# Performance work log

Measured on AMD Instinct MI355X. Metric: run time of the kernel, lower is better.

## Reference

```python
import jax, jax.numpy as jnp
import numpy as np

N_QUBITS = 10
DEPTH = 3
KSIZE = 16
DILATION = 1
NFREQ = 8

I4 = np.eye(4, dtype=np.complex64)
XX4 = np.fliplr(np.eye(4)).astype(np.complex64)
YY4 = np.array([[0, 0, 0, -1], [0, 0, 1, 0], [0, 1, 0, 0], [-1, 0, 0, 0]], dtype=np.complex64)


def _u3(t, p, l):
    ct = jnp.cos(t / 2).astype(jnp.complex64)
    st = jnp.sin(t / 2).astype(jnp.complex64)
    ep, el = jnp.exp(1j * p), jnp.exp(1j * l)
    return jnp.stack([jnp.stack([ct, -el * st]), jnp.stack([ep * st, ep * el * ct])])


def _ising_zz(t):
    em, ep = jnp.exp(-0.5j * t), jnp.exp(0.5j * t)
    return jnp.diag(jnp.stack([em, ep, ep, em]))


def _ising_xx(t):
    return jnp.cos(t / 2) * I4 - 1j * jnp.sin(t / 2) * XX4


def _ising_yy(t):
    return jnp.cos(t / 2) * I4 - 1j * jnp.sin(t / 2) * YY4


def _cu3(t, p, l):
    # controlled-U3 (control = 1): deferred-measurement form of qml.cond(measure, U3)
    return jnp.eye(4, dtype=jnp.complex64).at[2:, 2:].set(_u3(t, p, l))


def _apply_1q(state, U, wire):
    s = jnp.moveaxis(state, 1 + wire, -1)
    if U.ndim == 3:  # per-sample gate (batched angles)
        s = jnp.einsum('bij,b...j->b...i', U, s)
    else:
        s = jnp.einsum('ij,...j->...i', U, s)
    return jnp.moveaxis(s, -1, 1 + wire)


def _apply_2q(state, U, w1, w2):
    s = jnp.moveaxis(state, (1 + w1, 1 + w2), (-2, -1))
    shp = s.shape
    s = s.reshape(shp[:-2] + (4,))
    s = jnp.einsum('ij,...j->...i', U, s)
    return jnp.moveaxis(s.reshape(shp), (-2, -1), (1 + w1, 1 + w2))


def _run_circuit(angles, freq_scale, conv_params, pool_params):
    Bm = angles.shape[0]
    state = jnp.zeros((Bm, 2 ** N_QUBITS), jnp.complex64).at[:, 0].set(1.0)
    state = state.reshape((Bm,) + (2,) * N_QUBITS)
    # frequency-matched encoding: RY(a) then RX(freq_scale * a), per-sample angles
    for i in range(N_QUBITS):
        a = angles[:, i]
        c = jnp.cos(a / 2).astype(jnp.complex64)
        s = jnp.sin(a / 2).astype(jnp.complex64)
        ry = jnp.stack([jnp.stack([c, -s], -1), jnp.stack([s, c], -1)], -2)
        state = _apply_1q(state, ry, i)
        b = freq_scale[i] * a
        cb = jnp.cos(b / 2).astype(jnp.complex64)
        sb = jnp.sin(b / 2).astype(jnp.complex64)
        rx = jnp.stack([jnp.stack([cb, -1j * sb], -1), jnp.stack([-1j * sb, cb], -1)], -2)
        state = _apply_1q(state, rx, i)
    wires = list(range(N_QUBITS))
    for layer in range(DEPTH):
        wp = conv_params[layer]
        nw = len(wires)
        for parity in (0, 1):
            for i2, w in enumerate(wires):
                if i2 % 2 == parity and i2 < nw - 1:
                    nxt = wires[i2 + 1]
                    state = _apply_1q(state, _u3(wp[i2, 0], wp[i2, 1], wp[i2, 2]), w)
                    state = _apply_1q(state, _u3(wp[i2 + 1, 3], wp[i2 + 1, 4], wp[i2 + 1, 5]), nxt)
                    state = _apply_2q(state, _ising_zz(wp[i2, 6]), w, nxt)
                    state = _apply_2q(state, _ising_yy(wp[i2, 7]), w, nxt)
                    state = _apply_2q(state, _ising_xx(wp[i2, 8]), w, nxt)
                    state = _apply_1q(state, _u3(wp[i2, 9], wp[i2, 10], wp[i2, 11]), w)
                    state = _apply_1q(state, _u3(wp[i2 + 1, 12], wp[i2 + 1, 13], wp[i2 + 1, 14]), nxt)
        pp = pool_params[layer]
        for i2, w in enumerate(wires):
            if i2 % 2 == 1:
                state = _apply_2q(state, _cu3(pp[i2 // 2, 0], pp[i2 // 2, 1], pp[i2 // 2, 2]), w, wires[i2 - 1])
        wires = wires[::2]
    p = jnp.abs(state) ** 2
    p = p.reshape(Bm, 2, -1).sum(-1)
    return p[:, 0] - p[:, 1]  # <Z_0>


def _forward(x, proj_w, proj_b, freq_scale, conv_params, pool_params, agg_weights):
    B, C, T = x.shape
    eff = DILATION * (KSIZE - 1)
    W = T - eff
    idx = jnp.arange(W)[:, None] + DILATION * jnp.arange(KSIZE)[None, :]  # [W,K]
    win = x[:, :, idx]  # [B,C,W,K]
    f = jnp.fft.rfft(win, axis=-1)[..., :NFREQ]  # [B,C,W,NF]
    feats = jnp.stack([jnp.log1p(jnp.abs(f)), jnp.angle(f) / jnp.pi], -1)  # [B,C,W,NF,2]
    feats = jnp.transpose(feats, (0, 2, 1, 3, 4)).reshape(B, W, -1)  # [B,W,C*NF*2]
    proj = jnp.tanh(feats @ proj_w.T + proj_b) * jnp.pi  # [B,W,n_qubits]
    ev = _run_circuit(proj.reshape(B * W, N_QUBITS), freq_scale, conv_params, pool_params)
    outs = ev.reshape(B, W)
    wts = jax.nn.softmax(agg_weights[:W])
    return (outs * wts[None, :]).sum(1)


def setup_inputs():
    key = jax.random.key(0)
    k = jax.random.split(key, 6)
    fft_dim = 22 * NFREQ * 2
    return {
        'x': jax.random.normal(k[0], (16, 22, 128), jnp.float32),
        'proj_w': jax.random.normal(k[1], (N_QUBITS, fft_dim), jnp.float32) / np.sqrt(fft_dim).astype(np.float32),
        'proj_b': jnp.zeros((N_QUBITS,), jnp.float32),
        'freq_scale': jnp.linspace(0.5, 3.0, N_QUBITS, dtype=jnp.float32),
        'conv_params': 0.1 * jax.random.normal(k[2], (DEPTH, N_QUBITS, 15), jnp.float32),
        'pool_params': 0.1 * jax.random.normal(k[3], (DEPTH, N_QUBITS // 2, 3), jnp.float32),
        'agg_weights': jnp.zeros((113,), jnp.float32),
    }


def reference(x, proj_w, proj_b, freq_scale, conv_params, pool_params, agg_weights):
    return _forward(x, proj_w, proj_b, freq_scale, conv_params, pool_params, agg_weights)
```

## Files before the change

### kernel.cpp

```cpp
#include <hip/hip_runtime.h>
#include <math.h>

#define NQ 10
#define NSTATE 1024
#define WW 113
#define BB 16
#define CC 22
#define KK 16
#define NF 8
#define FDIM 352
#define NS (BB*WW)
#define NGATE 23
#define SL(j) ((j) ^ (((j) >> 5) & 31))

__device__ __forceinline__ float2 cmul(float2 a, float2 b) {
    return make_float2(a.x*b.x - a.y*b.y, a.x*b.y + a.y*b.x);
}

__constant__ int G_KIND[NGATE]  = {0,0,0,0,0, 0,0,0,0, 1,1,1,1,1, 0,0,0,0, 1,1, 0,0, 1};
__constant__ int G_LAYER[NGATE] = {0,0,0,0,0, 0,0,0,0, 0,0,0,0,0, 1,1,1,1, 1,1, 2,2, 2};
__constant__ int G_IA[NGATE]    = {0,2,4,6,8, 1,3,5,7, 0,1,2,3,4, 0,2,1,3, 0,1, 0,1, 0};

__device__ void u3mat(float2* U, float th, float ph, float lm) {
    float ct, st, cp, sp, cl, sl;
    sincosf(th * 0.5f, &st, &ct);
    sincosf(ph, &sp, &cp);
    sincosf(lm, &sl, &cl);
    U[0] = make_float2(ct, 0.f);
    U[1] = make_float2(-cl * st, -sl * st);
    U[2] = make_float2(cp * st, sp * st);
    U[3] = make_float2((cp * cl - sp * sl) * ct, (sp * cl + cp * sl) * ct);
}

__device__ void mm4(float2* C, const float2* A, const float2* B) {
#pragma unroll
    for (int i = 0; i < 4; ++i)
#pragma unroll
        for (int j = 0; j < 4; ++j) {
            float2 acc = make_float2(0.f, 0.f);
#pragma unroll
            for (int k = 0; k < 4; ++k) {
                float2 p = cmul(A[i*4+k], B[k*4+j]);
                acc.x += p.x; acc.y += p.y;
            }
            C[i*4+j] = acc;
        }
}

__global__ __launch_bounds__(64) void prep_kernel(
    const float* __restrict__ conv,
    const float* __restrict__ pool,
    const float* __restrict__ aggw,
    float2* __restrict__ mats,
    float* __restrict__ wts,
    float* __restrict__ out)
{
    const int t = threadIdx.x;

    float a0 = (t < WW) ? aggw[t] : -1e30f;
    float a1 = (t + 64 < WW) ? aggw[t + 64] : -1e30f;
    float mx = fmaxf(a0, a1);
    for (int off = 32; off > 0; off >>= 1) mx = fmaxf(mx, __shfl_xor(mx, off));
    float e0 = (t < WW) ? expf(a0 - mx) : 0.f;
    float e1 = (t + 64 < WW) ? expf(a1 - mx) : 0.f;
    float es = e0 + e1;
    for (int off = 32; off > 0; off >>= 1) es += __shfl_xor(es, off);
    float inv = 1.0f / es;
    if (t < WW) wts[t] = e0 * inv;
    if (t + 64 < WW) wts[t + 64] = e1 * inv;
    if (t < BB) out[t] = 0.f;

    if (t >= NGATE) return;
    int kind = G_KIND[t], layer = G_LAYER[t], ia = G_IA[t];
    float2 F[16];
    if (kind == 0) {
        const float* wp = conv + layer * 150;
        float2 Uw0[4], Un0[4], Uw1[4], Un1[4];
        u3mat(Uw0, wp[ia*15+0], wp[ia*15+1], wp[ia*15+2]);
        u3mat(Un0, wp[(ia+1)*15+3], wp[(ia+1)*15+4], wp[(ia+1)*15+5]);
        u3mat(Uw1, wp[ia*15+9], wp[ia*15+10], wp[ia*15+11]);
        u3mat(Un1, wp[(ia+1)*15+12], wp[(ia+1)*15+13], wp[(ia+1)*15+14]);
        float2 Kpre[16], Kpost[16];
#pragma unroll
        for (int a = 0; a < 2; ++a)
#pragma unroll
        for (int b = 0; b < 2; ++b)
#pragma unroll
        for (int c = 0; c < 2; ++c)
#pragma unroll
        for (int d = 0; d < 2; ++d) {
            Kpre [(2*a+b)*4 + (2*c+d)] = cmul(Uw0[a*2+c], Un0[b*2+d]);
            Kpost[(2*a+b)*4 + (2*c+d)] = cmul(Uw1[a*2+c], Un1[b*2+d]);
        }
        float cz, sz, cy, sy, cx, sx;
        sincosf(wp[ia*15+6] * 0.5f, &sz, &cz);
        sincosf(wp[ia*15+7] * 0.5f, &sy, &cy);
        sincosf(wp[ia*15+8] * 0.5f, &sx, &cx);
        float2 Z[16], Y[16], X[16];
#pragma unroll
        for (int k = 0; k < 16; ++k) { Z[k] = make_float2(0,0); Y[k] = make_float2(0,0); X[k] = make_float2(0,0); }
        Z[0]  = make_float2(cz, -sz); Z[5]  = make_float2(cz, sz);
        Z[10] = make_float2(cz,  sz); Z[15] = make_float2(cz, -sz);
        Y[0] = Y[5] = Y[10] = Y[15] = make_float2(cy, 0);
        Y[0*4+3] = make_float2(0,  sy); Y[1*4+2] = make_float2(0, -sy);
        Y[2*4+1] = make_float2(0, -sy); Y[3*4+0] = make_float2(0,  sy);
        X[0] = X[5] = X[10] = X[15] = make_float2(cx, 0);
        X[0*4+3] = X[1*4+2] = X[2*4+1] = X[3*4+0] = make_float2(0, -sx);
        float2 T1[16], M[16], T2[16];
        mm4(T1, Y, Z);
        mm4(M, X, T1);
        mm4(T2, M, Kpre);
        mm4(F, Kpost, T2);
    } else {
        const float* pp = pool + layer * 15 + ia * 3;
        float2 U[4];
        u3mat(U, pp[0], pp[1], pp[2]);
#pragma unroll
        for (int k = 0; k < 16; ++k) F[k] = make_float2(0,0);
        F[0*4+0] = make_float2(1,0); F[1*4+1] = make_float2(1,0);
        F[2*4+2] = U[0]; F[2*4+3] = U[1];
        F[3*4+2] = U[2]; F[3*4+3] = U[3];
    }
#pragma unroll
    for (int k = 0; k < 16; ++k) mats[t*16 + k] = F[k];
}

template<int PW, int PN>
__device__ __forceinline__ void gate2q(float2* st, const float2* __restrict__ m, int tid)
{
    constexpr int PL = (PW < PN) ? PW : PN;
    constexpr int PH = (PW < PN) ? PN : PW;
    int t1   = ((tid >> PL) << (PL + 1)) | (tid & ((1 << PL) - 1));
    int base = ((t1  >> PH) << (PH + 1)) | (t1  & ((1 << PH) - 1));
    const int i0 = SL(base);
    const int i1 = SL(base | (1 << PN));
    const int i2 = SL(base | (1 << PW));
    const int i3 = SL(base | (1 << PW) | (1 << PN));
    float2 a[4];
    a[0] = st[i0]; a[1] = st[i1]; a[2] = st[i2]; a[3] = st[i3];
    float2 n[4];
#pragma unroll
    for (int g = 0; g < 4; ++g) {
        float accx = 0.f, accy = 0.f;
#pragma unroll
        for (int h = 0; h < 4; ++h) {
            float2 mm = m[g*4 + h];
            accx = fmaf(mm.x, a[h].x, accx);
            accx = fmaf(-mm.y, a[h].y, accx);
            accy = fmaf(mm.x, a[h].y, accy);
            accy = fmaf(mm.y, a[h].x, accy);
        }
        n[g] = make_float2(accx, accy);
    }
    st[i0] = n[0]; st[i1] = n[1]; st[i2] = n[2]; st[i3] = n[3];
}

__global__ __launch_bounds__(256) void fused_kernel(
    const float* __restrict__ x,
    const float* __restrict__ proj_w,
    const float* __restrict__ proj_b,
    const float* __restrict__ freq_scale,
    const float2* __restrict__ mats,
    const float* __restrict__ wts,
    float* __restrict__ out)
{
    const int s = blockIdx.x;
    const int b = s / WW, w = s % WW;
    const int tid = threadIdx.x;

    __shared__ float2 st[NSTATE];
    __shared__ float twre[16], twim[16];
    __shared__ float angs[NQ];
    __shared__ float2 vq[2 * NQ];
    __shared__ float part[4];

    float* win  = (float*)st;
    float* feat = (float*)st + 512;

    for (int e = tid; e < CC * KK; e += 256) {
        int c = e >> 4, n = e & 15;
        win[e] = x[b * (CC * 128) + c * 128 + w + n];
    }
    if (tid < 16) {
        float ang = -(float)M_PI * (float)tid / 8.0f;
        twre[tid] = cosf(ang);
        twim[tid] = sinf(ang);
    }
    __syncthreads();

    float fval = 0.f, fval2 = 0.f;
    if (tid < CC * NF) {
        int c = tid >> 3, k = tid & 7;
        float re = 0.f, im = 0.f;
#pragma unroll
        for (int n = 0; n < 16; ++n) {
            int m = (k * n) & 15;
            float xv = win[c * 16 + n];
            re += xv * twre[m];
            im += xv * twim[m];
        }
        fval  = log1pf(sqrtf(re * re + im * im));
        fval2 = atan2f(im, re) * (float)(1.0 / M_PI);
    }
    __syncthreads();
    if (tid < CC * NF) {
        int c = tid >> 3, k = tid & 7;
        feat[c * 16 + k * 2]     = fval;
        feat[c * 16 + k * 2 + 1] = fval2;
    }
    __syncthreads();

    {
        int v = tid >> 6, lane = tid & 63;
        for (int q = v; q < NQ; q += 4) {
            float acc = 0.f;
            for (int e = lane; e < FDIM; e += 64) acc += feat[e] * proj_w[q * FDIM + e];
            for (int off = 32; off > 0; off >>= 1) acc += __shfl_xor(acc, off);
            if (lane == 0) angs[q] = tanhf(acc + proj_b[q]) * (float)M_PI;
        }
    }
    __syncthreads();

    if (tid < NQ) {
        float a = angs[tid];
        float bf = freq_scale[tid] * a;
        float ca, sa, cb, sb;
        sincosf(a * 0.5f, &sa, &ca);
        sincosf(bf * 0.5f, &sb, &cb);
        vq[2 * tid]     = make_float2(cb * ca, -sb * sa);
        vq[2 * tid + 1] = make_float2(cb * sa, -sb * ca);
    }
    __syncthreads();

    for (int idx = tid; idx < NSTATE; idx += 256) {
        float r = 1.f, i = 0.f;
#pragma unroll
        for (int q = 0; q < NQ; ++q) {
            int bit = (idx >> (9 - q)) & 1;
            float2 vv = vq[2 * q + bit];
            float nr = r * vv.x - i * vv.y;
            float ni = r * vv.y + i * vv.x;
            r = nr; i = ni;
        }
        st[SL(idx)] = make_float2(r, i);
    }
    __syncthreads();

#define GATE(G, PW, PN) gate2q<PW, PN>(st, mats + (G)*16, tid); __syncthreads();
    GATE(0, 9, 8) GATE(1, 7, 6) GATE(2, 5, 4) GATE(3, 3, 2) GATE(4, 1, 0)
    GATE(5, 8, 7) GATE(6, 6, 5) GATE(7, 4, 3) GATE(8, 2, 1)
    GATE(9, 8, 9) GATE(10, 6, 7) GATE(11, 4, 5) GATE(12, 2, 3) GATE(13, 0, 1)
    GATE(14, 9, 7) GATE(15, 5, 3) GATE(16, 7, 5) GATE(17, 3, 1)
    GATE(18, 7, 9) GATE(19, 3, 5)
    GATE(20, 9, 5) GATE(21, 5, 1)
    GATE(22, 5, 9)
#undef GATE

    float local = 0.f;
    for (int idx = tid; idx < NSTATE; idx += 256) {
        float2 am = st[idx];
        float p = am.x * am.x + am.y * am.y;
        local += (idx < 512) ? p : -p;
    }
    for (int off = 32; off > 0; off >>= 1) local += __shfl_xor(local, off);
    if ((tid & 63) == 0) part[tid >> 6] = local;
    __syncthreads();
    if (tid == 0) {
        float ev = part[0] + part[1] + part[2] + part[3];
        atomicAdd(&out[b], ev * wts[w]);
    }
}

extern "C" void kernel_launch(void* const* d_in, const int* in_sizes, int n_in,
                              void* d_out, int out_size, void* d_ws, size_t ws_size,
                              hipStream_t stream)
{
    const float* x           = (const float*)d_in[0];
    const float* proj_w      = (const float*)d_in[1];
    const float* proj_b      = (const float*)d_in[2];
    const float* freq_scale  = (const float*)d_in[3];
    const float* conv_params = (const float*)d_in[4];
    const float* pool_params = (const float*)d_in[5];
    const float* aggw        = (const float*)d_in[6];
    float* out = (float*)d_out;

    float2* mats = (float2*)d_ws;
    float* wts   = (float*)d_ws + NGATE * 16 * 2;

    prep_kernel<<<1, 64, 0, stream>>>(conv_params, pool_params, aggw, mats, wts, out);
    fused_kernel<<<NS, 256, 0, stream>>>(x, proj_w, proj_b, freq_scale, mats, wts, out);
}
```

Measured before the change: 112.0 us.

## Specialize controlled pooling gates and parallelize gate-matrix prep per element

Pooling gates are controlled-U3, so they now touch only the two amplitudes where the control bit is set, which halves shared-memory traffic and arithmetic for those gates. The gate-matrix prep kernel now uses one thread per matrix element, with a closed-form product, instead of one thread per gate doing several 4x4 matrix multiplies. Swizzled index offsets are derived by XOR instead of being recomputed, and the DFT uses fma. Block count and sync structure are unchanged, so the gain is limited to the gate phase and prep latency.

```diff
diff --git a/kernel.cpp b/kernel.cpp
--- a/kernel.cpp
+++ b/kernel.cpp
@@ -6,22 +6,31 @@
 #define WW 113
 #define BB 16
 #define CC 22
-#define KK 16
 #define NF 8
 #define FDIM 352
 #define NS (BB*WW)
 #define NGATE 23
-#define SL(j) ((j) ^ (((j) >> 5) & 31))
-
-__device__ __forceinline__ float2 cmul(float2 a, float2 b) {
+
+__device__ __forceinline__ constexpr int SLOT(int j) { return j ^ ((j >> 5) & 31); }
+__device__ __forceinline__ constexpr int DD(int p) { return (1 << p) | (p >= 5 ? (1 << (p - 5)) : 0); }
+
+__device__ __forceinline__ int ins0(int j, int p) {
+    return ((j >> p) << (p + 1)) | (j & ((1 << p) - 1));
+}
+
+__device__ __forceinline__ float2 cmulf(float2 a, float2 b) {
     return make_float2(a.x*b.x - a.y*b.y, a.x*b.y + a.y*b.x);
+}
+__device__ __forceinline__ void cmacf(float2& acc, float2 c, float2 v) {
+    acc.x = fmaf(c.x, v.x, acc.x); acc.x = fmaf(-c.y, v.y, acc.x);
+    acc.y = fmaf(c.x, v.y, acc.y); acc.y = fmaf(c.y, v.x, acc.y);
 }
 
 __constant__ int G_KIND[NGATE]  = {0,0,0,0,0, 0,0,0,0, 1,1,1,1,1, 0,0,0,0, 1,1, 0,0, 1};
 __constant__ int G_LAYER[NGATE] = {0,0,0,0,0, 0,0,0,0, 0,0,0,0,0, 1,1,1,1, 1,1, 2,2, 2};
 __constant__ int G_IA[NGATE]    = {0,2,4,6,8, 1,3,5,7, 0,1,2,3,4, 0,2,1,3, 0,1, 0,1, 0};
 
-__device__ void u3mat(float2* U, float th, float ph, float lm) {
+__device__ __forceinline__ void u3mat(float2* U, float th, float ph, float lm) {
     float ct, st, cp, sp, cl, sl;
     sincosf(th * 0.5f, &st, &ct);
     sincosf(ph, &sp, &cp);
@@ -32,22 +41,7 @@
     U[3] = make_float2((cp * cl - sp * sl) * ct, (sp * cl + cp * sl) * ct);
 }
 
-__device__ void mm4(float2* C, const float2* A, const float2* B) {
-#pragma unroll
-    for (int i = 0; i < 4; ++i)
-#pragma unroll
-        for (int j = 0; j < 4; ++j) {
-            float2 acc = make_float2(0.f, 0.f);
-#pragma unroll
-            for (int k = 0; k < 4; ++k) {
-                float2 p = cmul(A[i*4+k], B[k*4+j]);
-                acc.x += p.x; acc.y += p.y;
-            }
-            C[i*4+j] = acc;
-        }
-}
-
-__global__ __launch_bounds__(64) void prep_kernel(
+__global__ __launch_bounds__(384) void prep_kernel(
     const float* __restrict__ conv,
     const float* __restrict__ pool,
     const float* __restrict__ aggw,
@@ -57,102 +51,105 @@
 {
     const int t = threadIdx.x;
 
-    float a0 = (t < WW) ? aggw[t] : -1e30f;
-    float a1 = (t + 64 < WW) ? aggw[t + 64] : -1e30f;
-    float mx = fmaxf(a0, a1);
-    for (int off = 32; off > 0; off >>= 1) mx = fmaxf(mx, __shfl_xor(mx, off));
-    float e0 = (t < WW) ? expf(a0 - mx) : 0.f;
-    float e1 = (t + 64 < WW) ? expf(a1 - mx) : 0.f;
-    float es = e0 + e1;
-    for (int off = 32; off > 0; off >>= 1) es += __shfl_xor(es, off);
-    float inv = 1.0f / es;
-    if (t < WW) wts[t] = e0 * inv;
-    if (t + 64 < WW) wts[t + 64] = e1 * inv;
-    if (t < BB) out[t] = 0.f;
-
-    if (t >= NGATE) return;
-    int kind = G_KIND[t], layer = G_LAYER[t], ia = G_IA[t];
-    float2 F[16];
-    if (kind == 0) {
+    if (t < 64) {
+        float a0 = (t < WW) ? aggw[t] : -1e30f;
+        float a1 = (t + 64 < WW) ? aggw[t + 64] : -1e30f;
+        float mx = fmaxf(a0, a1);
+        for (int off = 32; off > 0; off >>= 1) mx = fmaxf(mx, __shfl_xor(mx, off));
+        float e0 = (t < WW) ? expf(a0 - mx) : 0.f;
+        float e1 = (t + 64 < WW) ? expf(a1 - mx) : 0.f;
+        float es = e0 + e1;
+        for (int off = 32; off > 0; off >>= 1) es += __shfl_xor(es, off);
+        float inv = 1.0f / es;
+        if (t < WW) wts[t] = e0 * inv;
+        if (t + 64 < WW) wts[t + 64] = e1 * inv;
+        if (t < BB) out[t] = 0.f;
+    }
+
+    if (t >= NGATE * 16) return;
+    const int g = t >> 4, k = t & 15;
+    const int i = k >> 2, j = k & 3;
+    const int kind = G_KIND[g], layer = G_LAYER[g], ia = G_IA[g];
+    float2 F;
+    if (kind == 1) {
+        const float* pp = pool + layer * 15 + ia * 3;
+        if (i < 2 || j < 2) {
+            F = (i == j) ? make_float2(1.f, 0.f) : make_float2(0.f, 0.f);
+        } else {
+            float2 U[4];
+            u3mat(U, pp[0], pp[1], pp[2]);
+            F = U[(i - 2) * 2 + (j - 2)];
+        }
+    } else {
         const float* wp = conv + layer * 150;
         float2 Uw0[4], Un0[4], Uw1[4], Un1[4];
-        u3mat(Uw0, wp[ia*15+0], wp[ia*15+1], wp[ia*15+2]);
-        u3mat(Un0, wp[(ia+1)*15+3], wp[(ia+1)*15+4], wp[(ia+1)*15+5]);
-        u3mat(Uw1, wp[ia*15+9], wp[ia*15+10], wp[ia*15+11]);
+        u3mat(Uw0, wp[ia*15+0],  wp[ia*15+1],  wp[ia*15+2]);
+        u3mat(Un0, wp[(ia+1)*15+3],  wp[(ia+1)*15+4],  wp[(ia+1)*15+5]);
+        u3mat(Uw1, wp[ia*15+9],  wp[ia*15+10], wp[ia*15+11]);
         u3mat(Un1, wp[(ia+1)*15+12], wp[(ia+1)*15+13], wp[(ia+1)*15+14]);
-        float2 Kpre[16], Kpost[16];
-#pragma unroll
-        for (int a = 0; a < 2; ++a)
-#pragma unroll
-        for (int b = 0; b < 2; ++b)
-#pragma unroll
-        for (int c = 0; c < 2; ++c)
-#pragma unroll
-        for (int d = 0; d < 2; ++d) {
-            Kpre [(2*a+b)*4 + (2*c+d)] = cmul(Uw0[a*2+c], Un0[b*2+d]);
-            Kpost[(2*a+b)*4 + (2*c+d)] = cmul(Uw1[a*2+c], Un1[b*2+d]);
-        }
         float cz, sz, cy, sy, cx, sx;
         sincosf(wp[ia*15+6] * 0.5f, &sz, &cz);
         sincosf(wp[ia*15+7] * 0.5f, &sy, &cy);
         sincosf(wp[ia*15+8] * 0.5f, &sx, &cx);
-        float2 Z[16], Y[16], X[16];
-#pragma unroll
-        for (int k = 0; k < 16; ++k) { Z[k] = make_float2(0,0); Y[k] = make_float2(0,0); X[k] = make_float2(0,0); }
-        Z[0]  = make_float2(cz, -sz); Z[5]  = make_float2(cz, sz);
-        Z[10] = make_float2(cz,  sz); Z[15] = make_float2(cz, -sz);
-        Y[0] = Y[5] = Y[10] = Y[15] = make_float2(cy, 0);
-        Y[0*4+3] = make_float2(0,  sy); Y[1*4+2] = make_float2(0, -sy);
-        Y[2*4+1] = make_float2(0, -sy); Y[3*4+0] = make_float2(0,  sy);
-        X[0] = X[5] = X[10] = X[15] = make_float2(cx, 0);
-        X[0*4+3] = X[1*4+2] = X[2*4+1] = X[3*4+0] = make_float2(0, -sx);
-        float2 T1[16], M[16], T2[16];
-        mm4(T1, Y, Z);
-        mm4(M, X, T1);
-        mm4(T2, M, Kpre);
-        mm4(F, Kpost, T2);
-    } else {
-        const float* pp = pool + layer * 15 + ia * 3;
-        float2 U[4];
-        u3mat(U, pp[0], pp[1], pp[2]);
-#pragma unroll
-        for (int k = 0; k < 16; ++k) F[k] = make_float2(0,0);
-        F[0*4+0] = make_float2(1,0); F[1*4+1] = make_float2(1,0);
-        F[2*4+2] = U[0]; F[2*4+3] = U[1];
-        F[3*4+2] = U[2]; F[3*4+3] = U[3];
-    }
-#pragma unroll
-    for (int k = 0; k < 16; ++k) mats[t*16 + k] = F[k];
+        float2 acc = make_float2(0.f, 0.f);
+#pragma unroll
+        for (int a = 0; a < 4; ++a) {
+            const float sa = (a == 0 || a == 3) ? 1.f : -1.f;
+            const float2 za = (a == 0 || a == 3) ? make_float2(cz, -sz)
+                                                 : make_float2(cz,  sz);
+            const float daa = fmaf(sa * sx, sy, cx * cy);
+            const float oaa = fmaf(sa * sy, cx, -sx * cy);
+            float2 Mdiag = make_float2(daa * za.x, daa * za.y);
+            float2 Moff  = make_float2(-oaa * za.y, oaa * za.x);
+            float2 kpost = cmulf(Uw1[(i >> 1) * 2 + (a >> 1)], Un1[(i & 1) * 2 + (a & 1)]);
+            float2 kpreA = cmulf(Uw0[(a >> 1) * 2 + (j >> 1)], Un0[(a & 1) * 2 + (j & 1)]);
+            float2 kpreN = cmulf(Uw0[(1 - (a >> 1)) * 2 + (j >> 1)], Un0[(1 - (a & 1)) * 2 + (j & 1)]);
+            float2 inner = cmulf(Mdiag, kpreA);
+            cmacf(inner, Moff, kpreN);
+            cmacf(acc, kpost, inner);
+        }
+        F = acc;
+    }
+    mats[g * 16 + k] = F;
 }
 
 template<int PW, int PN>
-__device__ __forceinline__ void gate2q(float2* st, const float2* __restrict__ m, int tid)
+__device__ __forceinline__ void conv2q(float2* st, const float2* __restrict__ m, int tid)
 {
     constexpr int PL = (PW < PN) ? PW : PN;
     constexpr int PH = (PW < PN) ? PN : PW;
     int t1   = ((tid >> PL) << (PL + 1)) | (tid & ((1 << PL) - 1));
     int base = ((t1  >> PH) << (PH + 1)) | (t1  & ((1 << PH) - 1));
-    const int i0 = SL(base);
-    const int i1 = SL(base | (1 << PN));
-    const int i2 = SL(base | (1 << PW));
-    const int i3 = SL(base | (1 << PW) | (1 << PN));
-    float2 a[4];
-    a[0] = st[i0]; a[1] = st[i1]; a[2] = st[i2]; a[3] = st[i3];
+    const int i0 = SLOT(base);
+    const int i1 = i0 ^ DD(PN);
+    const int i2 = i0 ^ DD(PW);
+    const int i3 = i2 ^ DD(PN);
+    float2 a0 = st[i0], a1 = st[i1], a2 = st[i2], a3 = st[i3];
     float2 n[4];
 #pragma unroll
     for (int g = 0; g < 4; ++g) {
-        float accx = 0.f, accy = 0.f;
-#pragma unroll
-        for (int h = 0; h < 4; ++h) {
-            float2 mm = m[g*4 + h];
-            accx = fmaf(mm.x, a[h].x, accx);
-            accx = fmaf(-mm.y, a[h].y, accx);
-            accy = fmaf(mm.x, a[h].y, accy);
-            accy = fmaf(mm.y, a[h].x, accy);
-        }
-        n[g] = make_float2(accx, accy);
+        float2 acc = cmulf(m[g*4+0], a0);
+        cmacf(acc, m[g*4+1], a1);
+        cmacf(acc, m[g*4+2], a2);
+        cmacf(acc, m[g*4+3], a3);
+        n[g] = acc;
     }
     st[i0] = n[0]; st[i1] = n[1]; st[i2] = n[2]; st[i3] = n[3];
+}
+
+template<int PC, int PT>
+__device__ __forceinline__ void pool2q(float2* st, const float2* __restrict__ m, int tid)
+{
+    constexpr int PL = (PC < PT) ? PC : PT;
+    constexpr int PH = (PC < PT) ? PT : PC;
+    int t1   = ((tid >> PL) << (PL + 1)) | (tid & ((1 << PL) - 1));
+    int base = ((t1  >> PH) << (PH + 1)) | (t1  & ((1 << PH) - 1));
+    const int i2 = SLOT(base) ^ DD(PC);
+    const int i3 = i2 ^ DD(PT);
+    float2 a2 = st[i2], a3 = st[i3];
+    float2 n2 = cmulf(m[10], a2); cmacf(n2, m[11], a3);
+    float2 n3 = cmulf(m[14], a2); cmacf(n3, m[15], a3);
+    st[i2] = n2; st[i3] = n3;
 }
 
 __global__ __launch_bounds__(256) void fused_kernel(
@@ -177,14 +174,14 @@
     float* win  = (float*)st;
     float* feat = (float*)st + 512;
 
-    for (int e = tid; e < CC * KK; e += 256) {
+    for (int e = tid; e < CC * 16; e += 256) {
         int c = e >> 4, n = e & 15;
         win[e] = x[b * (CC * 128) + c * 128 + w + n];
     }
     if (tid < 16) {
-        float ang = -(float)M_PI * (float)tid / 8.0f;
-        twre[tid] = cosf(ang);
-        twim[tid] = sinf(ang);
+        float ang = -(float)M_PI * (float)tid * 0.125f;
+        float sv, cv; sincosf(ang, &sv, &cv);
+        twre[tid] = cv; twim[tid] = sv;
     }
     __syncthreads();
 
@@ -194,10 +191,10 @@
         float re = 0.f, im = 0.f;
 #pragma unroll
         for (int n = 0; n < 16; ++n) {
-            int m = (k * n) & 15;
+            int mm = (k * n) & 15;
             float xv = win[c * 16 + n];
-            re += xv * twre[m];
-            im += xv * twim[m];
+            re = fmaf(xv, twre[mm], re);
+            im = fmaf(xv, twim[mm], im);
         }
         fval  = log1pf(sqrtf(re * re + im * im));
         fval2 = atan2f(im, re) * (float)(1.0 / M_PI);
@@ -205,8 +202,8 @@
     __syncthreads();
     if (tid < CC * NF) {
         int c = tid >> 3, k = tid & 7;
-        feat[c * 16 + k * 2]     = fval;
-        feat[c * 16 + k * 2 + 1] = fval2;
+        feat[c * 16 + (k << 1)]     = fval;
+        feat[c * 16 + (k << 1) + 1] = fval2;
     }
     __syncthreads();
 
@@ -242,19 +239,21 @@
             float ni = r * vv.y + i * vv.x;
             r = nr; i = ni;
         }
-        st[SL(idx)] = make_float2(r, i);
-    }
-    __syncthreads();
-
-#define GATE(G, PW, PN) gate2q<PW, PN>(st, mats + (G)*16, tid); __syncthreads();
-    GATE(0, 9, 8) GATE(1, 7, 6) GATE(2, 5, 4) GATE(3, 3, 2) GATE(4, 1, 0)
-    GATE(5, 8, 7) GATE(6, 6, 5) GATE(7, 4, 3) GATE(8, 2, 1)
-    GATE(9, 8, 9) GATE(10, 6, 7) GATE(11, 4, 5) GATE(12, 2, 3) GATE(13, 0, 1)
-    GATE(14, 9, 7) GATE(15, 5, 3) GATE(16, 7, 5) GATE(17, 3, 1)
-    GATE(18, 7, 9) GATE(19, 3, 5)
-    GATE(20, 9, 5) GATE(21, 5, 1)
-    GATE(22, 5, 9)
-#undef GATE
+        st[SLOT(idx)] = make_float2(r, i);
+    }
+    __syncthreads();
+
+#define CONV(G, PW, PN) conv2q<PW, PN>(st, mats + (G)*16, tid); __syncthreads();
+#define POOL(G, PC, PT) pool2q<PC, PT>(st, mats + (G)*16, tid); __syncthreads();
+    CONV(0, 9, 8) CONV(1, 7, 6) CONV(2, 5, 4) CONV(3, 3, 2) CONV(4, 1, 0)
+    CONV(5, 8, 7) CONV(6, 6, 5) CONV(7, 4, 3) CONV(8, 2, 1)
+    POOL(9, 8, 9) POOL(10, 6, 7) POOL(11, 4, 5) POOL(12, 2, 3) POOL(13, 0, 1)
+    CONV(14, 9, 7) CONV(15, 5, 3) CONV(16, 7, 5) CONV(17, 3, 1)
+    POOL(18, 7, 9) POOL(19, 3, 5)
+    CONV(20, 9, 5) CONV(21, 5, 1)
+    POOL(22, 5, 9)
+#undef CONV
+#undef POOL
 
     float local = 0.f;
     for (int idx = tid; idx < NSTATE; idx += 256) {
@@ -287,6 +286,6 @@
     float2* mats = (float2*)d_ws;
     float* wts   = (float*)d_ws + NGATE * 16 * 2;
 
-    prep_kernel<<<1, 64, 0, stream>>>(conv_params, pool_params, aggw, mats, wts, out);
+    prep_kernel<<<1, 384, 0, stream>>>(conv_params, pool_params, aggw, mats, wts, out);
     fused_kernel<<<NS, 256, 0, stream>>>(x, proj_w, proj_b, freq_scale, mats, wts, out);
 }
```

Result: slower. 120.0 us (+7.1%).
